# Kernel tuning notes

Measured on AMD Instinct MI355X. Metric: run time of the kernel, lower is better.

Reference implementation:

```python
import jax, jax.numpy as jnp
import numpy as np

HARDLIM_THRESH = 0.2


def setup_inputs() -> dict:
    key = jax.random.key(0)
    k_inp, k_w1, k_b1, k_w2, k_b2 = jax.random.split(key, 5)
    B, D, H, F = 16384, 4096, 2048, 512
    scale1 = 1.0 / np.sqrt(D)
    scale2 = 1.0 / np.sqrt(H)
    return {
        "inp": jax.random.normal(k_inp, (B, D), dtype=jnp.float32),
        "W1": jax.random.normal(k_w1, (H, D), dtype=jnp.float32) * scale1,
        "b1": jax.random.normal(k_b1, (H,), dtype=jnp.float32) * scale1,
        "W2": jax.random.normal(k_w2, (F, H), dtype=jnp.float32) * scale2,
        "b2": jax.random.normal(k_b2, (F,), dtype=jnp.float32) * scale2,
        "k": 8,
    }


def reference(inp, W1, b1, W2, b2, k):
    # Linear -> ReLU -> Linear
    h = jax.nn.relu(inp @ W1.T + b1)            # [B, H]
    logits = h @ W2.T + b2                      # [B, F]
    # 'hard' attention: sigmoid -> keep top-k (zero the rest) -> hardlim(0.2)
    s = jax.nn.sigmoid(logits)
    topk_vals, _ = jax.lax.top_k(s, k)          # [B, k]
    kth = topk_vals[:, -1:]                     # per-row k-th largest value
    gated = jnp.where(s >= kth, s, 0.0)         # GetTopK: zero non-top-k entries
    out = jnp.where(gated > HARDLIM_THRESH, 1.0, 0.0).astype(inp.dtype)
    return out
```

## Files before the change

kernel.cpp:

```cpp
#include <hip/hip_runtime.h>
#include <math.h>
#include <type_traits>


#define BM 128
#define BN 128
#define BK 16
#define BKF 32

#define TAU   1.0e-4f
#define L02F -1.3862943611198906f

typedef __attribute__((ext_vector_type(8))) short  bf16x8;
typedef __attribute__((ext_vector_type(8))) ushort u16x8;
typedef __attribute__((ext_vector_type(4))) float  f32x4;

__device__ inline ushort bfhi(float f)   { return (ushort)(__float_as_uint(f) >> 16); }
__device__ inline float  bfhif(float f)  { return __uint_as_float(__float_as_uint(f) & 0xFFFF0000u); }

__device__ inline void gload_lds16(const void* g, void* l) {
    __builtin_amdgcn_global_load_lds(
        (const __attribute__((address_space(1))) unsigned int*)g,
        (__attribute__((address_space(3))) unsigned int*)l, 16, 0, 0);
}

__global__ __launch_bounds__(256) void split_kernel(
    const float* __restrict__ src, ushort* __restrict__ hi,
    ushort* __restrict__ lo, size_t n4)
{
    size_t i = (size_t)blockIdx.x * 256 + threadIdx.x;
    size_t stride = (size_t)gridDim.x * 256;
    for (; i < n4; i += stride) {
        float4 v = ((const float4*)src)[i];
        ushort4 h, l;
        h.x = bfhi(v.x); l.x = bfhi(v.x - bfhif(v.x));
        h.y = bfhi(v.y); l.y = bfhi(v.y - bfhif(v.y));
        h.z = bfhi(v.z); l.z = bfhi(v.z - bfhif(v.z));
        h.w = bfhi(v.w); l.w = bfhi(v.w - bfhif(v.w));
        ((ushort4*)hi)[i] = h;
        ((ushort4*)lo)[i] = l;
    }
}

__global__ __launch_bounds__(512, 2) void bgemm1_8p(
    const float* __restrict__ inp,
    const ushort* __restrict__ w1h, const ushort* __restrict__ w1l,
    const float* __restrict__ b1,
    ushort* __restrict__ Chi, ushort* __restrict__ Clo)
{
    __shared__ ushort lds[73728];
    const int t    = threadIdx.x;
    const int lane = t & 63;
    const int wave = t >> 6;
    const int wr   = wave >> 1;
    const int wc   = wave & 1;
    const int l15  = lane & 15;
    const int l4   = lane >> 4;

    const int bid = blockIdx.x;
    const int xcd = bid & 7;
    const int j   = bid >> 3;
    const int bm  = xcd * 8 + (j >> 4);
    const int bn  = j & 15;

    const int ra  = t >> 1;
    const int kh  = t & 1;
    const int rb  = t >> 2;
    const int kqb = (t & 3) ^ (rb & 3);

    const float*  Abase = inp + ((size_t)(bm * 256 + ra)) * 4096 + kh * 16;
    const ushort* Bsh   = w1h + ((size_t)(bn * 128 + rb)) * 4096 + kqb * 8;
    const ushort* Bsl   = w1l + ((size_t)(bn * 128 + rb)) * 4096 + kqb * 8;

    f32x4 acc[4][4];
    #pragma unroll
    for (int mi = 0; mi < 4; ++mi)
        #pragma unroll
        for (int ni = 0; ni < 4; ++ni)
            acc[mi][ni] = (f32x4){0.f, 0.f, 0.f, 0.f};

    auto a_write = [&](int b, const f32x4 av[4]) {
        ushort h[16], l[16];
        #pragma unroll
        for (int i = 0; i < 4; ++i) {
            #pragma unroll
            for (int jj = 0; jj < 4; ++jj) {
                float x = av[i][jj];
                h[i * 4 + jj] = bfhi(x);
                l[i * 4 + jj] = bfhi(x - bfhif(x));
            }
        }
        ushort* A0 = &lds[b * 24576 + ra * 32];
        #pragma unroll
        for (int jj = 0; jj < 2; ++jj) {
            int u = (((2 * kh + jj) ^ (ra & 3)) << 3);
            *(u16x8*)&A0[u]        = *(const u16x8*)&h[jj * 8];
            *(u16x8*)&A0[8192 + u] = *(const u16x8*)&l[jj * 8];
        }
    };
    auto w_issue = [&](int b, int kt) {
        gload_lds16(Bsh + (size_t)kt * 32, &lds[b * 24576 + 16384 + wave * 512]);
        gload_lds16(Bsl + (size_t)kt * 32, &lds[b * 24576 + 20480 + wave * 512]);
    };
    auto a_load_asm = [&](int kt, f32x4 av[4]) {
        const float* p = Abase + (size_t)kt * 32;
        asm volatile("global_load_dwordx4 %0, %1, off"           : "=v"(av[0]) : "v"(p));
        asm volatile("global_load_dwordx4 %0, %1, off offset:16" : "=v"(av[1]) : "v"(p));
        asm volatile("global_load_dwordx4 %0, %1, off offset:32" : "=v"(av[2]) : "v"(p));
        asm volatile("global_load_dwordx4 %0, %1, off offset:48" : "=v"(av[3]) : "v"(p));
    };
    auto frag_read = [&](int b, bf16x8 ah[4], bf16x8 al[4], bf16x8 bh[4], bf16x8 bl[4]) {
        const ushort* L0 = &lds[b * 24576];
        #pragma unroll
        for (int mi = 0; mi < 4; ++mi) {
            int row = wr * 64 + mi * 16 + l15;
            int o = row * 32 + ((l4 ^ (row & 3)) << 3);
            ah[mi] = *(const bf16x8*)&L0[o];
            al[mi] = *(const bf16x8*)&L0[8192 + o];
        }
        #pragma unroll
        for (int ni = 0; ni < 4; ++ni) {
            int row = wc * 64 + ni * 16 + l15;
            int o = row * 32 + ((l4 ^ (row & 3)) << 3);
            bh[ni] = *(const bf16x8*)&L0[16384 + o];
            bl[ni] = *(const bf16x8*)&L0[20480 + o];
        }
    };
    auto do_mfma = [&](bf16x8 ah[4], bf16x8 al[4], bf16x8 bh[4], bf16x8 bl[4]) {
        __builtin_amdgcn_s_setprio(1);
        #pragma unroll
        for (int mi = 0; mi < 4; ++mi)
            #pragma unroll
            for (int ni = 0; ni < 4; ++ni) {
                acc[mi][ni] = __builtin_amdgcn_mfma_f32_16x16x32_bf16(ah[mi], bh[ni], acc[mi][ni], 0, 0, 0);
                acc[mi][ni] = __builtin_amdgcn_mfma_f32_16x16x32_bf16(ah[mi], bl[ni], acc[mi][ni], 0, 0, 0);
                acc[mi][ni] = __builtin_amdgcn_mfma_f32_16x16x32_bf16(al[mi], bh[ni], acc[mi][ni], 0, 0, 0);
            }
        __builtin_amdgcn_s_setprio(0);
    };
    #define BAR_KEEP() asm volatile("s_waitcnt lgkmcnt(0)\n\ts_barrier" ::: "memory")

    f32x4 avA[4], avB[4];

    {
        f32x4 a0[4];
        #pragma unroll
        for (int i = 0; i < 4; ++i) a0[i] = *(const f32x4*)(Abase + i * 4);
        a_write(0, a0);
        w_issue(0, 0);
        a_load_asm(1, avA);
        __builtin_amdgcn_sched_barrier(0);
        w_issue(1, 1);
        __builtin_amdgcn_sched_barrier(0);
        asm volatile("s_waitcnt vmcnt(6)");
        BAR_KEEP();
    }

    const int nt = 128;

    auto tile_body = [&](int kt, f32x4 (&cons)[4], f32x4 (&prod)[4]) {
        const int cur = kt % 3, nb1 = (kt + 1) % 3, nb2 = (kt + 2) % 3;
        bf16x8 ah[4], al[4], bh[4], bl[4];
        frag_read(cur, ah, al, bh, bl);
        a_load_asm(kt + 2, prod);
        __builtin_amdgcn_sched_barrier(0);
        w_issue(nb2, kt + 2);
        __builtin_amdgcn_sched_barrier(0);
        asm volatile("s_waitcnt vmcnt(6)");
        asm volatile("" : "+v"(cons[0]), "+v"(cons[1]), "+v"(cons[2]), "+v"(cons[3]));
        __builtin_amdgcn_sched_barrier(0);
        a_write(nb1, cons);
        do_mfma(ah, al, bh, bl);
        BAR_KEEP();
    };

    for (int kt = 0; kt < nt - 2; kt += 2) {
        tile_body(kt,     avA, avB);
        tile_body(kt + 1, avB, avA);
    }
    {
        const int kt = nt - 2;
        bf16x8 ah[4], al[4], bh[4], bl[4];
        frag_read(kt % 3, ah, al, bh, bl);
        asm volatile("s_waitcnt vmcnt(0)");
        asm volatile("" : "+v"(avA[0]), "+v"(avA[1]), "+v"(avA[2]), "+v"(avA[3]));
        __builtin_amdgcn_sched_barrier(0);
        a_write((kt + 1) % 3, avA);
        do_mfma(ah, al, bh, bl);
        BAR_KEEP();
    }
    {
        bf16x8 ah[4], al[4], bh[4], bl[4];
        frag_read((nt - 1) % 3, ah, al, bh, bl);
        do_mfma(ah, al, bh, bl);
    }

    #pragma unroll
    for (int ni = 0; ni < 4; ++ni) {
        int col = bn * 128 + wc * 64 + ni * 16 + l15;
        float bv = b1[col];
        #pragma unroll
        for (int mi = 0; mi < 4; ++mi) {
            int rowb = bm * 256 + wr * 64 + mi * 16 + l4 * 4;
            #pragma unroll
            for (int r = 0; r < 4; ++r) {
                float v = fmaxf(acc[mi][ni][r] + bv, 0.0f);
                size_t idx = (size_t)(rowb + r) * 2048 + col;
                Chi[idx] = bfhi(v);
                Clo[idx] = bfhi(v - bfhif(v));
            }
        }
    }
    #undef BAR_KEEP
}

template<int A_PRESPLIT, int W_PRESPLIT, int OUT_MODE>
__global__ __launch_bounds__(256) void bgemm_split(
    const float*  __restrict__ A32,
    const ushort* __restrict__ Ahg, const ushort* __restrict__ Alg, int lda,
    const float*  __restrict__ W32,
    const ushort* __restrict__ Whg, const ushort* __restrict__ Wlg, int ldw,
    const float*  __restrict__ bias,
    ushort* __restrict__ Chi, ushort* __restrict__ Clo,
    float*  __restrict__ C32, int N, int K)
{
    __shared__ __align__(16) ushort Ah[BM * BKF];
    __shared__ __align__(16) ushort Al[BM * BKF];
    __shared__ __align__(16) ushort Bh[BN * BKF];
    __shared__ __align__(16) ushort Bl[BN * BKF];

    const int t    = threadIdx.x;
    const int lane = t & 63;
    const int wave = t >> 6;
    const int wr   = wave >> 1;
    const int wc   = wave & 1;
    const int l15  = lane & 15;
    const int l4   = lane >> 4;
    const size_t bm = blockIdx.x;
    const size_t bn = blockIdx.y;

    f32x4 acc[4][4];
    #pragma unroll
    for (int mi = 0; mi < 4; ++mi)
        #pragma unroll
        for (int ni = 0; ni < 4; ++ni)
            acc[mi][ni] = (f32x4){0.f, 0.f, 0.f, 0.f};

    for (int k0 = 0; k0 < K; k0 += BKF) {
        if (A_PRESPLIT) {
            #pragma unroll
            for (int i = 0; i < 2; ++i) {
                int c = t + i * 256;
                int row = c >> 2, q = c & 3;
                size_t g = (bm * BM + row) * (size_t)lda + k0 + q * 8;
                *(uint4*)&Ah[row * BKF + q * 8] = *(const uint4*)(Ahg + g);
                *(uint4*)&Al[row * BKF + q * 8] = *(const uint4*)(Alg + g);
            }
        } else {
            #pragma unroll
            for (int i = 0; i < 4; ++i) {
                int c = t + i * 256;
                int row = c >> 3, q = c & 7;
                float4 v = *(const float4*)(A32 + (bm * BM + row) * (size_t)lda + k0 + q * 4);
                ushort4 h, l;
                h.x = bfhi(v.x); l.x = bfhi(v.x - bfhif(v.x));
                h.y = bfhi(v.y); l.y = bfhi(v.y - bfhif(v.y));
                h.z = bfhi(v.z); l.z = bfhi(v.z - bfhif(v.z));
                h.w = bfhi(v.w); l.w = bfhi(v.w - bfhif(v.w));
                *(ushort4*)&Ah[row * BKF + q * 4] = h;
                *(ushort4*)&Al[row * BKF + q * 4] = l;
            }
        }
        if (W_PRESPLIT) {
            #pragma unroll
            for (int i = 0; i < 2; ++i) {
                int c = t + i * 256;
                int row = c >> 2, q = c & 3;
                size_t g = (bn * BN + row) * (size_t)ldw + k0 + q * 8;
                *(uint4*)&Bh[row * BKF + q * 8] = *(const uint4*)(Whg + g);
                *(uint4*)&Bl[row * BKF + q * 8] = *(const uint4*)(Wlg + g);
            }
        } else {
            #pragma unroll
            for (int i = 0; i < 4; ++i) {
                int c = t + i * 256;
                int row = c >> 3, q = c & 7;
                float4 v = *(const float4*)(W32 + (bn * BN + row) * (size_t)ldw + k0 + q * 4);
                ushort4 h, l;
                h.x = bfhi(v.x); l.x = bfhi(v.x - bfhif(v.x));
                h.y = bfhi(v.y); l.y = bfhi(v.y - bfhif(v.y));
                h.z = bfhi(v.z); l.z = bfhi(v.z - bfhif(v.z));
                h.w = bfhi(v.w); l.w = bfhi(v.w - bfhif(v.w));
                *(ushort4*)&Bh[row * BKF + q * 4] = h;
                *(ushort4*)&Bl[row * BKF + q * 4] = l;
            }
        }
        __syncthreads();

        bf16x8 ah[4], al[4], bh[4], bl[4];
        #pragma unroll
        for (int mi = 0; mi < 4; ++mi) {
            int r = wr * 64 + mi * 16 + l15;
            ah[mi] = *(const bf16x8*)&Ah[r * BKF + l4 * 8];
            al[mi] = *(const bf16x8*)&Al[r * BKF + l4 * 8];
        }
        #pragma unroll
        for (int ni = 0; ni < 4; ++ni) {
            int r = wc * 64 + ni * 16 + l15;
            bh[ni] = *(const bf16x8*)&Bh[r * BKF + l4 * 8];
            bl[ni] = *(const bf16x8*)&Bl[r * BKF + l4 * 8];
        }
        #pragma unroll
        for (int mi = 0; mi < 4; ++mi)
            #pragma unroll
            for (int ni = 0; ni < 4; ++ni) {
                acc[mi][ni] = __builtin_amdgcn_mfma_f32_16x16x32_bf16(ah[mi], bh[ni], acc[mi][ni], 0, 0, 0);
                acc[mi][ni] = __builtin_amdgcn_mfma_f32_16x16x32_bf16(ah[mi], bl[ni], acc[mi][ni], 0, 0, 0);
                acc[mi][ni] = __builtin_amdgcn_mfma_f32_16x16x32_bf16(al[mi], bh[ni], acc[mi][ni], 0, 0, 0);
            }
        __syncthreads();
    }

    #pragma unroll
    for (int ni = 0; ni < 4; ++ni) {
        int col = (int)bn * BN + wc * 64 + ni * 16 + l15;
        float bv = bias[col];
        #pragma unroll
        for (int mi = 0; mi < 4; ++mi) {
            int rowb = (int)bm * BM + wr * 64 + mi * 16 + l4 * 4;
            #pragma unroll
            for (int r = 0; r < 4; ++r) {
                float v = acc[mi][ni][r] + bv;
                size_t idx = (size_t)(rowb + r) * N + col;
                if (OUT_MODE == 0) {
                    v = fmaxf(v, 0.0f);
                    Chi[idx] = bfhi(v);
                    Clo[idx] = bfhi(v - bfhif(v));
                } else {
                    C32[idx] = v;
                }
            }
        }
    }
}

__global__ __launch_bounds__(256) void repair_r1(
    const float* __restrict__ inp,
    const float* __restrict__ W1, const float* __restrict__ b1,
    double* __restrict__ h64,
    const int* __restrict__ risky, const int* __restrict__ cnt, int maxr)
{
    int c = *cnt; if (c > maxr) c = maxr;
    const int by = blockIdx.y;
    if (by * 4 >= c) return;
    __shared__ float Xs[4][4096];
    const int t = threadIdx.x;

    int ridx[4];
    #pragma unroll
    for (int r = 0; r < 4; ++r) {
        int slot = by * 4 + r;
        ridx[r] = risky[slot < c ? slot : (c - 1)];
    }
    #pragma unroll
    for (int i = 0; i < 16; ++i) {
        int lin = t + i * 256;
        int r = lin >> 10, q = lin & 1023;
        *(float4*)&Xs[r][q * 4] = *(const float4*)(inp + (size_t)ridx[r] * 4096 + q * 4);
    }
    __syncthreads();

    const int n0 = blockIdx.x * 512 + t;
    const int n1 = n0 + 256;
    const float* w0 = W1 + (size_t)n0 * 4096;
    const float* w1 = W1 + (size_t)n1 * 4096;
    double acc[2][4] = {};

    for (int k = 0; k < 4096; k += 4) {
        float4 a0 = *(const float4*)(w0 + k);
        float4 a1 = *(const float4*)(w1 + k);
        float xr[4][4];
        #pragma unroll
        for (int r = 0; r < 4; ++r)
            *(float4*)&xr[r][0] = *(const float4*)&Xs[r][k];
        const float* ap0 = &a0.x;
        const float* ap1 = &a1.x;
        #pragma unroll
        for (int j = 0; j < 4; ++j) {
            double wd0 = (double)ap0[j];
            double wd1 = (double)ap1[j];
            #pragma unroll
            for (int r = 0; r < 4; ++r) {
                double xd = (double)xr[r][j];
                acc[0][r] = fma(wd0, xd, acc[0][r]);
                acc[1][r] = fma(wd1, xd, acc[1][r]);
            }
        }
    }

    double bv0 = (double)b1[n0], bv1 = (double)b1[n1];
    #pragma unroll
    for (int r = 0; r < 4; ++r) {
        int slot = by * 4 + r;
        if (slot < c) {
            h64[(size_t)slot * 2048 + n0] = fmax(acc[0][r] + bv0, 0.0);
            h64[(size_t)slot * 2048 + n1] = fmax(acc[1][r] + bv1, 0.0);
        }
    }
}

__global__ __launch_bounds__(256) void repair_r2(
    const double* __restrict__ h64,
    const float* __restrict__ W2, const float* __restrict__ b2,
    double* __restrict__ L64,
    const int* __restrict__ cnt, int maxr)
{
    int c = *cnt; if (c > maxr) c = maxr;
    const int by = blockIdx.y;
    if (by * 4 >= c) return;
    __shared__ double Xs[4][2048];
    const int t = threadIdx.x;

    #pragma unroll
    for (int i = 0; i < 16; ++i) {
        int lin = t + i * 256;
        int r = lin >> 10, q = lin & 1023;
        int slot = by * 4 + r; if (slot >= c) slot = c - 1;
        *(double2*)&Xs[r][q * 2] = *(const double2*)(h64 + (size_t)slot * 2048 + q * 2);
    }
    __syncthreads();

    const int n0 = t;
    const int n1 = t + 256;
    const float* w0 = W2 + (size_t)n0 * 2048;
    const float* w1 = W2 + (size_t)n1 * 2048;
    double acc[2][4] = {};

    for (int k = 0; k < 2048; k += 4) {
        float4 a0 = *(const float4*)(w0 + k);
        float4 a1 = *(const float4*)(w1 + k);
        double xr[4][4];
        #pragma unroll
        for (int r = 0; r < 4; ++r) {
            *(double2*)&xr[r][0] = *(const double2*)&Xs[r][k];
            *(double2*)&xr[r][2] = *(const double2*)&Xs[r][k + 2];
        }
        const float* ap0 = &a0.x;
        const float* ap1 = &a1.x;
        #pragma unroll
        for (int j = 0; j < 4; ++j) {
            double wd0 = (double)ap0[j];
            double wd1 = (double)ap1[j];
            #pragma unroll
            for (int r = 0; r < 4; ++r) {
                acc[0][r] = fma(wd0, xr[r][j], acc[0][r]);
                acc[1][r] = fma(wd1, xr[r][j], acc[1][r]);
            }
        }
    }

    double bv0 = (double)b2[n0], bv1 = (double)b2[n1];
    #pragma unroll
    for (int r = 0; r < 4; ++r) {
        int slot = by * 4 + r;
        if (slot < c) {
            L64[(size_t)slot * 512 + n0] = acc[0][r] + bv0;
            L64[(size_t)slot * 512 + n1] = acc[1][r] + bv1;
        }
    }
}

template<typename TA, int MODE>
__global__ __launch_bounds__(256, 1) void gemm64(
    const TA* __restrict__ A, int lda,
    const float* __restrict__ W, int ldw,
    const float* __restrict__ bias,
    double* __restrict__ out64, int N, int K)
{
    __shared__ double As[BK][BM + 2];
    __shared__ double Bs[BK][BN + 2];
    const int t  = threadIdx.x;
    const int tm = t >> 4;
    const int tn = t & 15;
    const size_t bm = blockIdx.x;
    const size_t bn = blockIdx.y;
    const TA*    Ab = A + bm * BM * (size_t)lda;
    const float* Wb = W + bn * BN * (size_t)ldw;

    double acc[8][8] = {};

    for (int k0 = 0; k0 < K; k0 += BK) {
        #pragma unroll
        for (int i = 0; i < 2; ++i) {
            int f   = t + i * 256;
            int row = f >> 2;
            int kc  = (f & 3) << 2;
            if constexpr (std::is_same<TA, double>::value) {
                double2 v0 = *(const double2*)(Ab + (size_t)row * lda + k0 + kc);
                double2 v1 = *(const double2*)(Ab + (size_t)row * lda + k0 + kc + 2);
                As[kc + 0][row] = v0.x; As[kc + 1][row] = v0.y;
                As[kc + 2][row] = v1.x; As[kc + 3][row] = v1.y;
            } else {
                float4 va = *(const float4*)(Ab + (size_t)row * lda + k0 + kc);
                As[kc + 0][row] = (double)va.x; As[kc + 1][row] = (double)va.y;
                As[kc + 2][row] = (double)va.z; As[kc + 3][row] = (double)va.w;
            }
            float4 vb = *(const float4*)(Wb + (size_t)row * ldw + k0 + kc);
            Bs[kc + 0][row] = (double)vb.x; Bs[kc + 1][row] = (double)vb.y;
            Bs[kc + 2][row] = (double)vb.z; Bs[kc + 3][row] = (double)vb.w;
        }
        __syncthreads();
        #pragma unroll
        for (int k = 0; k < BK; ++k) {
            double a[8], b[8];
            #pragma unroll
            for (int i = 0; i < 4; ++i) {
                *(double2*)&a[i * 2] = *(const double2*)&As[k][tm * 8 + i * 2];
                *(double2*)&b[i * 2] = *(const double2*)&Bs[k][tn * 8 + i * 2];
            }
            #pragma unroll
            for (int i = 0; i < 8; ++i)
                #pragma unroll
                for (int j = 0; j < 8; ++j)
                    acc[i][j] = fma(a[i], b[j], acc[i][j]);
        }
        __syncthreads();
    }

    double bv[8];
    if (MODE != 2) {
        #pragma unroll
        for (int j = 0; j < 8; ++j) bv[j] = (double)bias[bn * BN + tn * 8 + j];
    }

    #pragma unroll
    for (int i = 0; i < 8; ++i) {
        size_t row  = bm * BM + (size_t)tm * 8 + i;
        size_t base = row * (size_t)N + bn * BN + tn * 8;
        #pragma unroll
        for (int j = 0; j < 8; ++j) {
            double v = acc[i][j];
            if (MODE == 0) out64[base + j] = fmax(v + bv[j], 0.0);
            if (MODE == 1) out64[base + j] = v + bv[j];
            if (MODE == 2) out64[base + j] += v;
        }
    }
}

__global__ void init_repair(int* risky, int* cnt, int maxr)
{
    int i = blockIdx.x * 256 + threadIdx.x;
    if (i == 0) *cnt = 0;
    if (i < maxr) risky[i] = 0;
}

__global__ __launch_bounds__(256) void margin_topk32(
    const float* L, float* O, int ncols,
    const int* __restrict__ kp, int* __restrict__ risky, int* __restrict__ cnt,
    int maxr)
{
    const int wave = threadIdx.x >> 6;
    const int lane = threadIdx.x & 63;
    const int k = *kp;
    const size_t row = (size_t)blockIdx.x * 4 + wave;
    const float* Lr = L + row * (size_t)ncols;

    float v[8];
    *(float4*)&v[0] = *(const float4*)(Lr + lane * 8);
    *(float4*)&v[4] = *(const float4*)(Lr + lane * 8 + 4);
    float w[8];
    #pragma unroll
    for (int j = 0; j < 8; ++j) w[j] = v[j];

    float kth = -3.0e38f, minD = 3.0e38f;
    for (int it = 0; it < k; ++it) {
        float mv = w[0]; int mj = 0;
        #pragma unroll
        for (int j = 1; j < 8; ++j)
            if (w[j] > mv) { mv = w[j]; mj = j; }
        int mi = lane * 8 + mj;
        #pragma unroll
        for (int off = 32; off; off >>= 1) {
            float ov = __shfl_xor(mv, off);
            int   oi = __shfl_xor(mi, off);
            if (ov > mv || (ov == mv && oi < mi)) { mv = ov; mi = oi; }
        }
        kth = mv;
        minD = fminf(minD, fabsf(mv - L02F));
        if ((mi >> 3) == lane) w[mi & 7] = -3.0e38f;
    }
    float nv = w[0];
    #pragma unroll
    for (int j = 1; j < 8; ++j) nv = fmaxf(nv, w[j]);
    #pragma unroll
    for (int off = 32; off; off >>= 1) nv = fmaxf(nv, __shfl_xor(nv, off));

    bool risk = ((kth - nv) < 2.0f * TAU) || (minD < TAU);
    if (risk && lane == 0) {
        int p = atomicAdd(cnt, 1);
        if (p < maxr) risky[p] = (int)row;
    }

    float o[8];
    #pragma unroll
    for (int j = 0; j < 8; ++j)
        o[j] = (v[j] >= kth && v[j] > L02F) ? 1.0f : 0.0f;
    float* Op = O + row * (size_t)ncols + lane * 8;
    *(float4*)&Op[0] = *(const float4*)&o[0];
    *(float4*)&Op[4] = *(const float4*)&o[4];
}

__global__ __launch_bounds__(256) void topk64_kernel(
    const double* __restrict__ L, float* __restrict__ O, int ncols,
    const int* __restrict__ kp,
    const int* __restrict__ risky, const int* __restrict__ cnt, int maxr)
{
    const int wave = threadIdx.x >> 6;
    const int lane = threadIdx.x & 63;
    const int k = *kp;
    size_t pos = (size_t)blockIdx.x * 4 + wave;
    size_t row = pos;
    if (cnt) {
        int c = *cnt; if (c > maxr) c = maxr;
        if ((int)pos >= c) return;
        row = (size_t)risky[pos];
    }
    const double* Lr = L + pos * (size_t)ncols;

    double v[8];
    #pragma unroll
    for (int j = 0; j < 8; ++j) {
        double l = Lr[lane * 8 + j];
        v[j] = 1.0 / (1.0 + exp(-l));
    }
    double w[8];
    #pragma unroll
    for (int j = 0; j < 8; ++j) w[j] = v[j];

    double kth = -1.0e300;
    for (int it = 0; it < k; ++it) {
        double mv = w[0]; int mj = 0;
        #pragma unroll
        for (int j = 1; j < 8; ++j)
            if (w[j] > mv) { mv = w[j]; mj = j; }
        int mi = lane * 8 + mj;
        #pragma unroll
        for (int off = 32; off; off >>= 1) {
            double ov = __shfl_xor(mv, off);
            int    oi = __shfl_xor(mi, off);
            if (ov > mv || (ov == mv && oi < mi)) { mv = ov; mi = oi; }
        }
        kth = mv;
        if ((mi >> 3) == lane) w[mi & 7] = -1.0e300;
    }

    float o[8];
    #pragma unroll
    for (int j = 0; j < 8; ++j)
        o[j] = (v[j] >= kth && v[j] > 0.2) ? 1.0f : 0.0f;
    float* Op = O + row * (size_t)ncols + lane * 8;
    *(float4*)&Op[0] = *(const float4*)&o[0];
    *(float4*)&Op[4] = *(const float4*)&o[4];
}

extern "C" void kernel_launch(void* const* d_in, const int* in_sizes, int n_in,
                              void* d_out, int out_size, void* d_ws, size_t ws_size,
                              hipStream_t stream) {
    const float* inp = (const float*)d_in[0];
    const float* W1  = (const float*)d_in[1];
    const float* b1  = (const float*)d_in[2];
    const float* W2  = (const float*)d_in[3];
    const float* b2  = (const float*)d_in[4];
    const int*   kp  = (const int*)d_in[5];

    const int H = in_sizes[2];
    const int F = in_sizes[4];
    const int D = in_sizes[1] / H;
    const int B = in_sizes[0] / D;
    float* out = (float*)d_out;

    const int MAXR = 8192;
    const size_t szHpair = (size_t)B * H * 4;
    const size_t szW1p   = (size_t)H * D * 4;
    const size_t szW2p   = (size_t)F * H * 4;
    const size_t needMain = szHpair + szW1p + szW2p + (size_t)MAXR * 4 + 256;
    const bool shapeOK = (D == 4096 && H == 2048 && F == 512 && B == 16384);

    if (shapeOK && ws_size >= needMain) {
        ushort* h_hi  = (ushort*)d_ws;
        ushort* h_lo  = h_hi + (size_t)B * H;
        ushort* w1h   = (ushort*)((char*)d_ws + szHpair);
        ushort* w1l   = w1h + (size_t)H * D;
        ushort* w2h   = (ushort*)((char*)d_ws + szHpair + szW1p);
        ushort* w2l   = w2h + (size_t)F * H;
        int*    risky = (int*)((char*)d_ws + szHpair + szW1p + szW2p);
        int*    cnt   = risky + MAXR;
        double* h64   = (double*)d_ws;
        double* L64   = (double*)((char*)d_ws + szHpair);
        float*  l32   = out;

        init_repair<<<(MAXR + 255) / 256, 256, 0, stream>>>(risky, cnt, MAXR);
        split_kernel<<<2048, 256, 0, stream>>>(W1, w1h, w1l, (size_t)H * D / 4);
        split_kernel<<<512, 256, 0, stream>>>(W2, w2h, w2l, (size_t)F * H / 4);
        bgemm1_8p<<<1024, 512, 0, stream>>>(inp, w1h, w1l, b1, h_hi, h_lo);
        bgemm_split<1, 1, 1><<<dim3(B / BM, F / BN), 256, 0, stream>>>(
            nullptr, h_hi, h_lo, H, nullptr, w2h, w2l, H, b2,
            nullptr, nullptr, l32, F, H);
        margin_topk32<<<B / 4, 256, 0, stream>>>(l32, out, F, kp, risky, cnt, MAXR);
        repair_r1<<<dim3(4, MAXR / 4), 256, 0, stream>>>(
            inp, W1, b1, h64, risky, cnt, MAXR);
        repair_r2<<<dim3(1, MAXR / 4), 256, 0, stream>>>(
            h64, W2, b2, L64, cnt, MAXR);
        topk64_kernel<<<MAXR / 4, 256, 0, stream>>>(L64, out, F, kp, risky, cnt, MAXR);
    } else {
        int Hc = H, Bc = 0;
        for (;;) {
            size_t perRow = (size_t)F * 8 + (size_t)Hc * 8;
            Bc = (int)((ws_size / perRow) / BM) * BM;
            if (Bc >= BM || Hc <= BM) break;
            Hc >>= 1;
        }
        if (Bc < BM) Bc = BM;
        if (Bc > B)  Bc = B;
        double* L   = (double*)d_ws;
        double* h64 = L + (size_t)Bc * F;

        for (int b0 = 0; b0 < B; b0 += Bc) {
            int bc = (B - b0 < Bc) ? (B - b0) : Bc;
            for (int h0 = 0; h0 < H; h0 += Hc) {
                int hc = (H - h0 < Hc) ? (H - h0) : Hc;
                gemm64<float, 0><<<dim3(bc / BM, hc / BN), 256, 0, stream>>>(
                    inp + (size_t)b0 * D, D, W1 + (size_t)h0 * D, D, b1 + h0,
                    h64, hc, D);
                if (h0 == 0)
                    gemm64<double, 1><<<dim3(bc / BM, F / BN), 256, 0, stream>>>(
                        h64, hc, W2 + h0, H, b2, L, F, hc);
                else
                    gemm64<double, 2><<<dim3(bc / BM, F / BN), 256, 0, stream>>>(
                        h64, hc, W2 + h0, H, b2, L, F, hc);
            }
            topk64_kernel<<<bc / 4, 256, 0, stream>>>(
                L, out + (size_t)b0 * F, F, kp, nullptr, nullptr, 0);
        }
    }
}
```

Baseline: 1.421 ms.

## Pre-split input to bf16 pairs and use direct global-to-LDS GEMM for both layers

Adds a templated GEMM kernel that stages both A and W bf16 hi/lo tiles straight into LDS with global_load_lds and a triple-buffered pipeline. When the workspace is large enough, the fp32 input is split into hi/lo bf16 by a separate pass, so GEMM1 no longer converts A in registers. The second GEMM is moved from the simple synchronous kernel onto the same pipelined kernel with 256x128 tiles. It also changes the LDS swizzle to XOR with (row>>1)&3. The trade is an extra full read and write of the 256MB input for the split pass, against a leaner GEMM inner loop.

```diff
diff --git a/kernel.cpp b/kernel.cpp
--- a/kernel.cpp
+++ b/kernel.cpp
@@ -6,7 +6,6 @@
 #define BM 128
 #define BN 128
 #define BK 16
-#define BKF 32
 
 #define TAU   1.0e-4f
 #define L02F -1.3862943611198906f
@@ -42,11 +41,14 @@
     }
 }
 
-__global__ __launch_bounds__(512, 2) void bgemm1_8p(
-    const float* __restrict__ inp,
-    const ushort* __restrict__ w1h, const ushort* __restrict__ w1l,
-    const float* __restrict__ b1,
-    ushort* __restrict__ Chi, ushort* __restrict__ Clo)
+template<int OUT_SPLIT>
+__global__ __launch_bounds__(512, 2) void bgemm_glds(
+    const ushort* __restrict__ aH, const ushort* __restrict__ aL,
+    const ushort* __restrict__ wH, const ushort* __restrict__ wL,
+    const float* __restrict__ bias,
+    ushort* __restrict__ Chi, ushort* __restrict__ Clo,
+    float* __restrict__ C32,
+    int N, int K, int nbm, int nbn)
 {
     __shared__ ushort lds[73728];
     const int t    = threadIdx.x;
@@ -60,13 +62,142 @@
     const int bid = blockIdx.x;
     const int xcd = bid & 7;
     const int j   = bid >> 3;
+    const int bm  = xcd * (nbm >> 3) + j / nbn;
+    const int bn  = j % nbn;
+
+    const int c   = lane & 3;
+    const int rA0 = (wave * 2 + 0) * 16 + (lane >> 2);
+    const int rA1 = (wave * 2 + 1) * 16 + (lane >> 2);
+    const int rB  = wave * 16 + (lane >> 2);
+    const size_t offA0 = (size_t)(bm * 256 + rA0) * K + (size_t)((c ^ ((rA0 >> 1) & 3)) * 8);
+    const size_t offA1 = (size_t)(bm * 256 + rA1) * K + (size_t)((c ^ ((rA1 >> 1) & 3)) * 8);
+    const size_t offB  = (size_t)(bn * 128 + rB ) * K + (size_t)((c ^ ((rB  >> 1) & 3)) * 8);
+    const ushort* sAh0 = aH + offA0; const ushort* sAl0 = aL + offA0;
+    const ushort* sAh1 = aH + offA1; const ushort* sAl1 = aL + offA1;
+    const ushort* sBh  = wH + offB;  const ushort* sBl  = wL + offB;
+
+    f32x4 acc[4][4];
+    #pragma unroll
+    for (int mi = 0; mi < 4; ++mi)
+        #pragma unroll
+        for (int ni = 0; ni < 4; ++ni)
+            acc[mi][ni] = (f32x4){0.f, 0.f, 0.f, 0.f};
+
+    auto stage = [&](int b, int kt) {
+        const size_t ko = (size_t)kt * 32;
+        ushort* L0 = &lds[b * 24576];
+        gload_lds16(sAh0 + ko, L0 + (wave * 2 + 0) * 512);
+        gload_lds16(sAh1 + ko, L0 + (wave * 2 + 1) * 512);
+        gload_lds16(sAl0 + ko, L0 + 8192 + (wave * 2 + 0) * 512);
+        gload_lds16(sAl1 + ko, L0 + 8192 + (wave * 2 + 1) * 512);
+        gload_lds16(sBh + ko,  L0 + 16384 + wave * 512);
+        gload_lds16(sBl + ko,  L0 + 20480 + wave * 512);
+    };
+    auto frag_read = [&](int b, bf16x8 ah[4], bf16x8 al[4], bf16x8 bh[4], bf16x8 bl[4]) {
+        const ushort* L0 = &lds[b * 24576];
+        #pragma unroll
+        for (int mi = 0; mi < 4; ++mi) {
+            int row = wr * 64 + mi * 16 + l15;
+            int o = row * 32 + ((l4 ^ ((row >> 1) & 3)) << 3);
+            ah[mi] = *(const bf16x8*)&L0[o];
+            al[mi] = *(const bf16x8*)&L0[8192 + o];
+        }
+        #pragma unroll
+        for (int ni = 0; ni < 4; ++ni) {
+            int row = wc * 64 + ni * 16 + l15;
+            int o = row * 32 + ((l4 ^ ((row >> 1) & 3)) << 3);
+            bh[ni] = *(const bf16x8*)&L0[16384 + o];
+            bl[ni] = *(const bf16x8*)&L0[20480 + o];
+        }
+    };
+    auto do_mfma = [&](bf16x8 ah[4], bf16x8 al[4], bf16x8 bh[4], bf16x8 bl[4]) {
+        __builtin_amdgcn_s_setprio(1);
+        #pragma unroll
+        for (int mi = 0; mi < 4; ++mi)
+            #pragma unroll
+            for (int ni = 0; ni < 4; ++ni) {
+                acc[mi][ni] = __builtin_amdgcn_mfma_f32_16x16x32_bf16(ah[mi], bh[ni], acc[mi][ni], 0, 0, 0);
+                acc[mi][ni] = __builtin_amdgcn_mfma_f32_16x16x32_bf16(ah[mi], bl[ni], acc[mi][ni], 0, 0, 0);
+                acc[mi][ni] = __builtin_amdgcn_mfma_f32_16x16x32_bf16(al[mi], bh[ni], acc[mi][ni], 0, 0, 0);
+            }
+        __builtin_amdgcn_s_setprio(0);
+    };
+
+    stage(0, 0);
+    stage(1, 1);
+    asm volatile("s_waitcnt vmcnt(6)");
+    __builtin_amdgcn_s_barrier();
+
+    const int nt = K / 32;
+    bf16x8 ah[4], al[4], bh[4], bl[4];
+
+    for (int kt = 0; kt < nt - 2; ++kt) {
+        frag_read(kt % 3, ah, al, bh, bl);
+        stage((kt + 2) % 3, kt + 2);
+        __builtin_amdgcn_sched_barrier(0);
+        do_mfma(ah, al, bh, bl);
+        asm volatile("s_waitcnt vmcnt(6)");
+        asm volatile("s_waitcnt lgkmcnt(0)\n\ts_barrier" ::: "memory");
+    }
+    {
+        frag_read((nt - 2) % 3, ah, al, bh, bl);
+        do_mfma(ah, al, bh, bl);
+        asm volatile("s_waitcnt vmcnt(0)");
+        asm volatile("s_waitcnt lgkmcnt(0)\n\ts_barrier" ::: "memory");
+    }
+    {
+        frag_read((nt - 1) % 3, ah, al, bh, bl);
+        do_mfma(ah, al, bh, bl);
+    }
+
+    #pragma unroll
+    for (int ni = 0; ni < 4; ++ni) {
+        int col = bn * 128 + wc * 64 + ni * 16 + l15;
+        float bv = bias[col];
+        #pragma unroll
+        for (int mi = 0; mi < 4; ++mi) {
+            int rowb = bm * 256 + wr * 64 + mi * 16 + l4 * 4;
+            #pragma unroll
+            for (int r = 0; r < 4; ++r) {
+                float v = acc[mi][ni][r] + bv;
+                size_t idx = (size_t)(rowb + r) * N + col;
+                if (OUT_SPLIT) {
+                    v = fmaxf(v, 0.0f);
+                    Chi[idx] = bfhi(v);
+                    Clo[idx] = bfhi(v - bfhif(v));
+                } else {
+                    C32[idx] = v;
+                }
+            }
+        }
+    }
+}
+
+__global__ __launch_bounds__(512, 2) void bgemm1_8p(
+    const float* __restrict__ inp,
+    const ushort* __restrict__ w1h, const ushort* __restrict__ w1l,
+    const float* __restrict__ b1,
+    ushort* __restrict__ Chi, ushort* __restrict__ Clo)
+{
+    __shared__ ushort lds[73728];
+    const int t    = threadIdx.x;
+    const int lane = t & 63;
+    const int wave = t >> 6;
+    const int wr   = wave >> 1;
+    const int wc   = wave & 1;
+    const int l15  = lane & 15;
+    const int l4   = lane >> 4;
+
+    const int bid = blockIdx.x;
+    const int xcd = bid & 7;
+    const int j   = bid >> 3;
     const int bm  = xcd * 8 + (j >> 4);
     const int bn  = j & 15;
 
     const int ra  = t >> 1;
     const int kh  = t & 1;
     const int rb  = t >> 2;
-    const int kqb = (t & 3) ^ (rb & 3);
+    const int kqb = (t & 3) ^ ((rb >> 1) & 3);
 
     const float*  Abase = inp + ((size_t)(bm * 256 + ra)) * 4096 + kh * 16;
     const ushort* Bsh   = w1h + ((size_t)(bn * 128 + rb)) * 4096 + kqb * 8;
@@ -93,7 +224,7 @@
         ushort* A0 = &lds[b * 24576 + ra * 32];
         #pragma unroll
         for (int jj = 0; jj < 2; ++jj) {
-            int u = (((2 * kh + jj) ^ (ra & 3)) << 3);
+            int u = (((2 * kh + jj) ^ ((ra >> 1) & 3)) << 3);
             *(u16x8*)&A0[u]        = *(const u16x8*)&h[jj * 8];
             *(u16x8*)&A0[8192 + u] = *(const u16x8*)&l[jj * 8];
         }
@@ -114,14 +245,14 @@
         #pragma unroll
         for (int mi = 0; mi < 4; ++mi) {
             int row = wr * 64 + mi * 16 + l15;
-            int o = row * 32 + ((l4 ^ (row & 3)) << 3);
+            int o = row * 32 + ((l4 ^ ((row >> 1) & 3)) << 3);
             ah[mi] = *(const bf16x8*)&L0[o];
             al[mi] = *(const bf16x8*)&L0[8192 + o];
         }
         #pragma unroll
         for (int ni = 0; ni < 4; ++ni) {
             int row = wc * 64 + ni * 16 + l15;
-            int o = row * 32 + ((l4 ^ (row & 3)) << 3);
+            int o = row * 32 + ((l4 ^ ((row >> 1) & 3)) << 3);
             bh[ni] = *(const bf16x8*)&L0[16384 + o];
             bl[ni] = *(const bf16x8*)&L0[20480 + o];
         }
@@ -141,7 +272,6 @@
     #define BAR_KEEP() asm volatile("s_waitcnt lgkmcnt(0)\n\ts_barrier" ::: "memory")
 
     f32x4 avA[4], avB[4];
-
     {
         f32x4 a0[4];
         #pragma unroll
@@ -157,7 +287,6 @@
     }
 
     const int nt = 128;
-
     auto tile_body = [&](int kt, f32x4 (&cons)[4], f32x4 (&prod)[4]) {
         const int cur = kt % 3, nb1 = (kt + 1) % 3, nb2 = (kt + 2) % 3;
         bf16x8 ah[4], al[4], bh[4], bl[4];
@@ -214,136 +343,6 @@
     #undef BAR_KEEP
 }
 
-template<int A_PRESPLIT, int W_PRESPLIT, int OUT_MODE>
-__global__ __launch_bounds__(256) void bgemm_split(
-    const float*  __restrict__ A32,
-    const ushort* __restrict__ Ahg, const ushort* __restrict__ Alg, int lda,
-    const float*  __restrict__ W32,
-    const ushort* __restrict__ Whg, const ushort* __restrict__ Wlg, int ldw,
-    const float*  __restrict__ bias,
-    ushort* __restrict__ Chi, ushort* __restrict__ Clo,
-    float*  __restrict__ C32, int N, int K)
-{
-    __shared__ __align__(16) ushort Ah[BM * BKF];
-    __shared__ __align__(16) ushort Al[BM * BKF];
-    __shared__ __align__(16) ushort Bh[BN * BKF];
-    __shared__ __align__(16) ushort Bl[BN * BKF];
-
-    const int t    = threadIdx.x;
-    const int lane = t & 63;
-    const int wave = t >> 6;
-    const int wr   = wave >> 1;
-    const int wc   = wave & 1;
-    const int l15  = lane & 15;
-    const int l4   = lane >> 4;
-    const size_t bm = blockIdx.x;
-    const size_t bn = blockIdx.y;
-
-    f32x4 acc[4][4];
-    #pragma unroll
-    for (int mi = 0; mi < 4; ++mi)
-        #pragma unroll
-        for (int ni = 0; ni < 4; ++ni)
-            acc[mi][ni] = (f32x4){0.f, 0.f, 0.f, 0.f};
-
-    for (int k0 = 0; k0 < K; k0 += BKF) {
-        if (A_PRESPLIT) {
-            #pragma unroll
-            for (int i = 0; i < 2; ++i) {
-                int c = t + i * 256;
-                int row = c >> 2, q = c & 3;
-                size_t g = (bm * BM + row) * (size_t)lda + k0 + q * 8;
-                *(uint4*)&Ah[row * BKF + q * 8] = *(const uint4*)(Ahg + g);
-                *(uint4*)&Al[row * BKF + q * 8] = *(const uint4*)(Alg + g);
-            }
-        } else {
-            #pragma unroll
-            for (int i = 0; i < 4; ++i) {
-                int c = t + i * 256;
-                int row = c >> 3, q = c & 7;
-                float4 v = *(const float4*)(A32 + (bm * BM + row) * (size_t)lda + k0 + q * 4);
-                ushort4 h, l;
-                h.x = bfhi(v.x); l.x = bfhi(v.x - bfhif(v.x));
-                h.y = bfhi(v.y); l.y = bfhi(v.y - bfhif(v.y));
-                h.z = bfhi(v.z); l.z = bfhi(v.z - bfhif(v.z));
-                h.w = bfhi(v.w); l.w = bfhi(v.w - bfhif(v.w));
-                *(ushort4*)&Ah[row * BKF + q * 4] = h;
-                *(ushort4*)&Al[row * BKF + q * 4] = l;
-            }
-        }
-        if (W_PRESPLIT) {
-            #pragma unroll
-            for (int i = 0; i < 2; ++i) {
-                int c = t + i * 256;
-                int row = c >> 2, q = c & 3;
-                size_t g = (bn * BN + row) * (size_t)ldw + k0 + q * 8;
-                *(uint4*)&Bh[row * BKF + q * 8] = *(const uint4*)(Whg + g);
-                *(uint4*)&Bl[row * BKF + q * 8] = *(const uint4*)(Wlg + g);
-            }
-        } else {
-            #pragma unroll
-            for (int i = 0; i < 4; ++i) {
-                int c = t + i * 256;
-                int row = c >> 3, q = c & 7;
-                float4 v = *(const float4*)(W32 + (bn * BN + row) * (size_t)ldw + k0 + q * 4);
-                ushort4 h, l;
-                h.x = bfhi(v.x); l.x = bfhi(v.x - bfhif(v.x));
-                h.y = bfhi(v.y); l.y = bfhi(v.y - bfhif(v.y));
-                h.z = bfhi(v.z); l.z = bfhi(v.z - bfhif(v.z));
-                h.w = bfhi(v.w); l.w = bfhi(v.w - bfhif(v.w));
-                *(ushort4*)&Bh[row * BKF + q * 4] = h;
-                *(ushort4*)&Bl[row * BKF + q * 4] = l;
-            }
-        }
-        __syncthreads();
-
-        bf16x8 ah[4], al[4], bh[4], bl[4];
-        #pragma unroll
-        for (int mi = 0; mi < 4; ++mi) {
-            int r = wr * 64 + mi * 16 + l15;
-            ah[mi] = *(const bf16x8*)&Ah[r * BKF + l4 * 8];
-            al[mi] = *(const bf16x8*)&Al[r * BKF + l4 * 8];
-        }
-        #pragma unroll
-        for (int ni = 0; ni < 4; ++ni) {
-            int r = wc * 64 + ni * 16 + l15;
-            bh[ni] = *(const bf16x8*)&Bh[r * BKF + l4 * 8];
-            bl[ni] = *(const bf16x8*)&Bl[r * BKF + l4 * 8];
-        }
-        #pragma unroll
-        for (int mi = 0; mi < 4; ++mi)
-            #pragma unroll
-            for (int ni = 0; ni < 4; ++ni) {
-                acc[mi][ni] = __builtin_amdgcn_mfma_f32_16x16x32_bf16(ah[mi], bh[ni], acc[mi][ni], 0, 0, 0);
-                acc[mi][ni] = __builtin_amdgcn_mfma_f32_16x16x32_bf16(ah[mi], bl[ni], acc[mi][ni], 0, 0, 0);
-                acc[mi][ni] = __builtin_amdgcn_mfma_f32_16x16x32_bf16(al[mi], bh[ni], acc[mi][ni], 0, 0, 0);
-            }
-        __syncthreads();
-    }
-
-    #pragma unroll
-    for (int ni = 0; ni < 4; ++ni) {
-        int col = (int)bn * BN + wc * 64 + ni * 16 + l15;
-        float bv = bias[col];
-        #pragma unroll
-        for (int mi = 0; mi < 4; ++mi) {
-            int rowb = (int)bm * BM + wr * 64 + mi * 16 + l4 * 4;
-            #pragma unroll
-            for (int r = 0; r < 4; ++r) {
-                float v = acc[mi][ni][r] + bv;
-                size_t idx = (size_t)(rowb + r) * N + col;
-                if (OUT_MODE == 0) {
-                    v = fmaxf(v, 0.0f);
-                    Chi[idx] = bfhi(v);
-                    Clo[idx] = bfhi(v - bfhif(v));
-                } else {
-                    C32[idx] = v;
-                }
-            }
-        }
-    }
-}
-
 __global__ __launch_bounds__(256) void repair_r1(
     const float* __restrict__ inp,
     const float* __restrict__ W1, const float* __restrict__ b1,
@@ -683,7 +682,9 @@
     const size_t szHpair = (size_t)B * H * 4;
     const size_t szW1p   = (size_t)H * D * 4;
     const size_t szW2p   = (size_t)F * H * 4;
+    const size_t szInpP  = (size_t)B * D * 4;
     const size_t needMain = szHpair + szW1p + szW2p + (size_t)MAXR * 4 + 256;
+    const size_t needA    = needMain + szInpP;
     const bool shapeOK = (D == 4096 && H == 2048 && F == 512 && B == 16384);
 
     if (shapeOK && ws_size >= needMain) {
@@ -702,10 +703,19 @@
         init_repair<<<(MAXR + 255) / 256, 256, 0, stream>>>(risky, cnt, MAXR);
         split_kernel<<<2048, 256, 0, stream>>>(W1, w1h, w1l, (size_t)H * D / 4);
         split_kernel<<<512, 256, 0, stream>>>(W2, w2h, w2l, (size_t)F * H / 4);
-        bgemm1_8p<<<1024, 512, 0, stream>>>(inp, w1h, w1l, b1, h_hi, h_lo);
-        bgemm_split<1, 1, 1><<<dim3(B / BM, F / BN), 256, 0, stream>>>(
-            nullptr, h_hi, h_lo, H, nullptr, w2h, w2l, H, b2,
-            nullptr, nullptr, l32, F, H);
+
+        if (ws_size >= needA) {
+            ushort* inH = (ushort*)((char*)d_ws + needMain);
+            ushort* inL = inH + (size_t)B * D;
+            split_kernel<<<4096, 256, 0, stream>>>(inp, inH, inL, (size_t)B * D / 4);
+            bgemm_glds<1><<<1024, 512, 0, stream>>>(
+                inH, inL, w1h, w1l, b1, h_hi, h_lo, nullptr, H, D, B / 256, H / 128);
+        } else {
+            bgemm1_8p<<<1024, 512, 0, stream>>>(inp, w1h, w1l, b1, h_hi, h_lo);
+        }
+        bgemm_glds<0><<<256, 512, 0, stream>>>(
+            h_hi, h_lo, w2h, w2l, b2, nullptr, nullptr, l32, F, H, B / 256, F / 128);
+
         margin_topk32<<<B / 4, 256, 0, stream>>>(l32, out, F, kp, risky, cnt, MAXR);
         repair_r1<<<dim3(4, MAXR / 4), 256, 0, stream>>>(
             inp, W1, b1, h64, risky, cnt, MAXR);
```

Result: no change. 1.402 ms (-1.3%).
